# Optimization experiments

Measured on AMD Instinct MI355X. Metric: run time of the kernel, lower is better.

## Reference

```python
import jax, jax.numpy as jnp
import numpy as np

# --- constants from loss_param_dict (fallback norm_info: means=0, stds=1 -> denorm is identity) ---
A_DIV, A_NS, A_BC = 0.3, 0.3, 0.3
A_LOSS = 1.0 - A_DIV - A_NS - A_BC
SCALE_BASE, SCALE_DIV, SCALE_NS, SCALE_BC = 300000.0, 1e-05, 0.01, 1.0
SX, SY = 1.2 / 127, 0.8 / 127  # spacing along axis 2 (x) and axis 1 (y)
RHO, MU = 1.0, 1.0
H, W = 128, 128
IN_TOP = H // 2 + H // 16 + 1  # 73
IN_BOT = H // 2 - H // 16 - 1  # 55
NORM_MEAN = np.array([0.0, 0.0, 0.0, 0.0], dtype=np.float32)
NORM_STD = np.array([1.0, 1.0, 1.0, 1.0], dtype=np.float32)


def grad_axis(f, h, axis):
    """torch.gradient: 2nd-order central interior, 1st-order one-sided edges."""
    f = jnp.moveaxis(f, axis, -1)
    left = (f[..., 1:2] - f[..., 0:1]) / h
    interior = (f[..., 2:] - f[..., :-2]) / (2.0 * h)
    right = (f[..., -1:] - f[..., -2:-1]) / h
    g = jnp.concatenate([left, interior, right], axis=-1)
    return jnp.moveaxis(g, -1, axis)


def setup_inputs() -> dict:
    key = jax.random.key(0)
    k1, k2, k3 = jax.random.split(key, 3)
    B = 256
    return {
        "inputs": jax.random.normal(k1, (B, 1, H, W), dtype=jnp.float32),
        "outputs": jax.random.normal(k2, (B, 3, H, W), dtype=jnp.float32),
        "targets": jax.random.normal(k3, (B, 3, H, W), dtype=jnp.float32),
    }


def reference(inputs, outputs, targets):
    # base MSE loss (reduction='sum')
    loss_base = jnp.sum((outputs - targets) ** 2) / SCALE_BASE

    # denormalisation (norm_info fallback: identity, but kept for faithfulness)
    in_ch = inputs.shape[1]
    mean = jnp.asarray(NORM_MEAN)
    std = jnp.asarray(NORM_STD)
    inp = inputs * std[:in_ch][None, :, None, None] + mean[:in_ch][None, :, None, None]
    out = outputs * std[in_ch:][None, :, None, None] + mean[in_ch:][None, :, None, None]

    # boundary residual pieces (on full, un-cropped denormalised outputs)
    pieces = [
        out[:, 1, IN_BOT:IN_TOP, 0].ravel() - 0.01,
        out[:, 0, IN_BOT:IN_TOP, -1].ravel(),
    ]
    for ch in (1, 2):
        for idx in (0, -1):
            pieces += [
                out[:, ch, idx, :].ravel(),
                out[:, ch, IN_TOP:, idx].ravel(),
                out[:, ch, 0:IN_BOT, idx].ravel(),
            ]
    boundary = jnp.concatenate(pieces)

    # interior crop [B, C, 126, 126]
    i_loc = inp[:, :, 1 : H - 1, 1 : W - 1]
    o_loc = out[:, :, 1 : H - 1, 1 : W - 1]

    p, u, v = o_loc[:, 0], o_loc[:, 1], o_loc[:, 2]  # [B,126,126]
    alpha = i_loc[:, 0]

    dp_dx, dp_dy = grad_axis(p, SX, 2), grad_axis(p, SY, 1)
    du_dx, du_dy = grad_axis(u, SX, 2), grad_axis(u, SY, 1)
    dv_dx, dv_dy = grad_axis(v, SX, 2), grad_axis(v, SY, 1)
    du_dxx = grad_axis(du_dx, SX, 2)
    du_dyy = grad_axis(du_dy, SY, 1)
    dv_dxx = grad_axis(dv_dx, SX, 2)
    dv_dyy = grad_axis(dv_dy, SY, 1)

    # continuity residual
    loss_cont = jnp.mean((du_dx + dv_dy) ** 2) / SCALE_DIV

    # Navier-Stokes residual
    x_res = u * du_dx + v * du_dy + dp_dx / RHO - MU * (du_dxx + du_dyy) / RHO + alpha * u / RHO
    y_res = u * dv_dx + v * dv_dy + dp_dy / RHO - MU * (dv_dxx + dv_dyy) / RHO + alpha * v / RHO
    mse_ns = (jnp.mean(x_res**2, axis=(1, 2)) + jnp.mean(y_res**2, axis=(1, 2))).mean() / 2.0
    loss_ns = mse_ns / SCALE_NS

    # boundary residual
    loss_bc = jnp.mean(boundary**2) / SCALE_BC

    return A_LOSS * loss_base + A_DIV * loss_cont + A_NS * loss_ns + A_BC * loss_bc
```

## Files before the change

### kernel.cpp

```cpp
#include <hip/hip_runtime.h>


#define HH 128
#define WW 128
#define NI 126
#define NBLK 4096

template <int I> __device__ __forceinline__ float gc(const float4& f) {
    if constexpr (I == 0) return f.x;
    else if constexpr (I == 1) return f.y;
    else if constexpr (I == 2) return f.z;
    else return f.w;
}

template <int IDX>
__device__ __forceinline__ float xsel(const float4& l, const float4& m, const float4& r) {
    if constexpr (IDX < 4) return gc<IDX>(l);
    else if constexpr (IDX < 8) return gc<IDX - 4>(m);
    else return gc<IDX - 8>(r);
}

__device__ __forceinline__ float grad1s(float m1, float a0, float p1, int i,
                                        float inv_h, float inv_2h) {
    if (i == 0) return (p1 - a0) * inv_h;
    if (i == NI - 1) return (a0 - m1) * inv_h;
    return (p1 - m1) * inv_2h;
}

__device__ __forceinline__ float grad2s(float m2, float m1, float a0, float p1, float p2,
                                        int i, float inv_h, float inv_2h) {
    if (i == 0) {
        const float d1 = (p2 - a0) * inv_2h, d0 = (p1 - a0) * inv_h;
        return (d1 - d0) * inv_h;
    }
    if (i == 1) {
        const float d1 = (p2 - a0) * inv_2h, dm1 = (a0 - m1) * inv_h;
        return (d1 - dm1) * inv_2h;
    }
    if (i == NI - 1) {
        const float d0 = (a0 - m1) * inv_h, dm1 = (a0 - m2) * inv_2h;
        return (d0 - dm1) * inv_h;
    }
    if (i == NI - 2) {
        const float d1 = (p1 - a0) * inv_h, dm1 = (a0 - m2) * inv_2h;
        return (d1 - dm1) * inv_2h;
    }
    return (p2 - 2.f * a0 + m2) * inv_2h * inv_2h;
}

struct Acc { float base, bc, cont, ns; };

template <int Q>
__device__ __forceinline__ void do_pixel(
    int r, int c0, bool midrow,
    const float4& uxl, const float4& uxm, const float4& uxr,
    const float4& uym2, const float4& uym1, const float4& uyp1, const float4& uyp2,
    const float4& vxl, const float4& vxm, const float4& vxr,
    const float4& vym2, const float4& vym1, const float4& vyp1, const float4& vyp2,
    const float4& pxl, const float4& pxm, const float4& pxr,
    const float4& pym1, const float4& pyp1,
    const float4& t0, const float4& t1, const float4& t2, const float4& av,
    Acc& acc) {
    const int c = c0 + Q;
    const float u0 = xsel<Q + 4>(uxl, uxm, uxr);
    const float v0 = xsel<Q + 4>(vxl, vxm, vxr);
    const float p0 = xsel<Q + 4>(pxl, pxm, pxr);

    {
        const float d0 = p0 - gc<Q>(t0);
        const float d1 = u0 - gc<Q>(t1);
        const float d2 = v0 - gc<Q>(t2);
        acc.base += d0 * d0 + d1 * d1 + d2 * d2;
    }
    if (c == 0 && midrow) { const float d = u0 - 0.01f; acc.bc += d * d; }
    if (c == WW - 1 && midrow) { acc.bc += p0 * p0; }
    if (r == 0 || r == HH - 1) { acc.bc += u0 * u0 + v0 * v0; }
    if ((c == 0 || c == WW - 1) && !midrow) { acc.bc += u0 * u0 + v0 * v0; }

    if (r >= 1 && r <= HH - 2 && c >= 1 && c <= WW - 2) {
        const int ic = c - 1, ir = r - 1;
        const float inv_sx = 127.0f / 1.2f, inv_2sx = 127.0f / 2.4f;
        const float inv_sy = 127.0f / 0.8f, inv_2sy = 127.0f / 1.6f;

        const float uxm2 = xsel<Q + 2>(uxl, uxm, uxr), uxm1 = xsel<Q + 3>(uxl, uxm, uxr);
        const float uxp1 = xsel<Q + 5>(uxl, uxm, uxr), uxp2 = xsel<Q + 6>(uxl, uxm, uxr);
        const float vxm2 = xsel<Q + 2>(vxl, vxm, vxr), vxm1 = xsel<Q + 3>(vxl, vxm, vxr);
        const float vxp1 = xsel<Q + 5>(vxl, vxm, vxr), vxp2 = xsel<Q + 6>(vxl, vxm, vxr);
        const float pxm1 = xsel<Q + 3>(pxl, pxm, pxr), pxp1 = xsel<Q + 5>(pxl, pxm, pxr);
        const float uym2s = gc<Q>(uym2), uym1s = gc<Q>(uym1);
        const float uyp1s = gc<Q>(uyp1), uyp2s = gc<Q>(uyp2);
        const float vym2s = gc<Q>(vym2), vym1s = gc<Q>(vym1);
        const float vyp1s = gc<Q>(vyp1), vyp2s = gc<Q>(vyp2);
        const float pym1s = gc<Q>(pym1), pyp1s = gc<Q>(pyp1);

        const float du_dx = grad1s(uxm1, u0, uxp1, ic, inv_sx, inv_2sx);
        const float du_dy = grad1s(uym1s, u0, uyp1s, ir, inv_sy, inv_2sy);
        const float dv_dx = grad1s(vxm1, v0, vxp1, ic, inv_sx, inv_2sx);
        const float dv_dy = grad1s(vym1s, v0, vyp1s, ir, inv_sy, inv_2sy);
        const float dp_dx = grad1s(pxm1, p0, pxp1, ic, inv_sx, inv_2sx);
        const float dp_dy = grad1s(pym1s, p0, pyp1s, ir, inv_sy, inv_2sy);
        const float du_dxx = grad2s(uxm2, uxm1, u0, uxp1, uxp2, ic, inv_sx, inv_2sx);
        const float du_dyy = grad2s(uym2s, uym1s, u0, uyp1s, uyp2s, ir, inv_sy, inv_2sy);
        const float dv_dxx = grad2s(vxm2, vxm1, v0, vxp1, vxp2, ic, inv_sx, inv_2sx);
        const float dv_dyy = grad2s(vym2s, vym1s, v0, vyp1s, vyp2s, ir, inv_sy, inv_2sy);

        const float alpha = gc<Q>(av);
        const float dvg = du_dx + dv_dy;
        acc.cont += dvg * dvg;
        const float xr_ = u0 * du_dx + v0 * du_dy + dp_dx - (du_dxx + du_dyy) + alpha * u0;
        const float yr_ = u0 * dv_dx + v0 * dv_dy + dp_dy - (dv_dxx + dv_dyy) + alpha * v0;
        acc.ns += xr_ * xr_ + yr_ * yr_;
    }
}

__global__ __launch_bounds__(256, 4) void physics_loss_kernel(
    const float* __restrict__ inp, const float* __restrict__ out,
    const float* __restrict__ tgt, double* __restrict__ ws) {
    const int tid = threadIdx.x;
    const int grp = tid & 31;
    const int rloc = tid >> 5;
    const int bid = ((blockIdx.x & 7) << 9) | (blockIdx.x >> 3);
    const int b = bid >> 4;
    const int r = ((bid & 15) << 3) | rloc;
    const int c0 = grp << 2;

    const float* O = out + (size_t)b * 3 * HH * WW;
    const float* T = tgt + (size_t)b * 3 * HH * WW;
    const float* A = inp + (size_t)b * HH * WW;
    const float* P = O;
    const float* U = O + HH * WW;
    const float* V = O + 2 * HH * WW;

    const int gl = grp == 0 ? 0 : grp - 1;
    const int gr = grp == 31 ? 31 : grp + 1;
    const int rm2 = r < 2 ? 0 : r - 2;
    const int rm1 = r < 1 ? 0 : r - 1;
    const int rp1 = r > 126 ? 127 : r + 1;
    const int rp2 = r > 125 ? 127 : r + 2;

    auto ld = [&](const float* base, int row, int gg) {
        return reinterpret_cast<const float4*>(base + row * WW)[gg];
    };

    const float4 uxl = ld(U, r, gl), uxm = ld(U, r, grp), uxr = ld(U, r, gr);
    const float4 uym2 = ld(U, rm2, grp), uym1 = ld(U, rm1, grp);
    const float4 uyp1 = ld(U, rp1, grp), uyp2 = ld(U, rp2, grp);
    const float4 vxl = ld(V, r, gl), vxm = ld(V, r, grp), vxr = ld(V, r, gr);
    const float4 vym2 = ld(V, rm2, grp), vym1 = ld(V, rm1, grp);
    const float4 vyp1 = ld(V, rp1, grp), vyp2 = ld(V, rp2, grp);
    const float4 pxl = ld(P, r, gl), pxm = ld(P, r, grp), pxr = ld(P, r, gr);
    const float4 pym1 = ld(P, rm1, grp), pyp1 = ld(P, rp1, grp);
    const float4 t0 = ld(T, r, grp);
    const float4 t1 = ld(T + HH * WW, r, grp);
    const float4 t2 = ld(T + 2 * HH * WW, r, grp);
    const float4 av = ld(A, r, grp);
    __builtin_amdgcn_sched_barrier(0);

    const bool midrow = (r >= 55 && r < 73);
    Acc acc = {0.f, 0.f, 0.f, 0.f};

    do_pixel<0>(r, c0, midrow, uxl, uxm, uxr, uym2, uym1, uyp1, uyp2,
                vxl, vxm, vxr, vym2, vym1, vyp1, vyp2,
                pxl, pxm, pxr, pym1, pyp1, t0, t1, t2, av, acc);
    do_pixel<1>(r, c0, midrow, uxl, uxm, uxr, uym2, uym1, uyp1, uyp2,
                vxl, vxm, vxr, vym2, vym1, vyp1, vyp2,
                pxl, pxm, pxr, pym1, pyp1, t0, t1, t2, av, acc);
    do_pixel<2>(r, c0, midrow, uxl, uxm, uxr, uym2, uym1, uyp1, uyp2,
                vxl, vxm, vxr, vym2, vym1, vyp1, vyp2,
                pxl, pxm, pxr, pym1, pyp1, t0, t1, t2, av, acc);
    do_pixel<3>(r, c0, midrow, uxl, uxm, uxr, uym2, uym1, uyp1, uyp2,
                vxl, vxm, vxr, vym2, vym1, vyp1, vyp2,
                pxl, pxm, pxr, pym1, pyp1, t0, t1, t2, av, acc);

    float a_base = acc.base, a_bc = acc.bc, a_cont = acc.cont, a_ns = acc.ns;
    #pragma unroll
    for (int off = 32; off > 0; off >>= 1) {
        a_base += __shfl_down(a_base, off);
        a_bc   += __shfl_down(a_bc, off);
        a_cont += __shfl_down(a_cont, off);
        a_ns   += __shfl_down(a_ns, off);
    }
    __shared__ float red[4][4];
    const int wave = tid >> 6, lane = tid & 63;
    if (lane == 0) {
        red[wave][0] = a_base; red[wave][1] = a_bc;
        red[wave][2] = a_cont; red[wave][3] = a_ns;
    }
    __syncthreads();
    if (tid == 0) {
        double b0 = 0, b1 = 0, b2 = 0, b3 = 0;
        #pragma unroll
        for (int w = 0; w < 4; ++w) {
            b0 += red[w][0]; b1 += red[w][1]; b2 += red[w][2]; b3 += red[w][3];
        }
        double* slot = ws + (size_t)bid * 4;
        slot[0] = b0; slot[1] = b1; slot[2] = b2; slot[3] = b3;
    }
}

__global__ __launch_bounds__(256) void finalize_kernel(const double* __restrict__ ws,
                                                       float* __restrict__ out) {
    const int tid = threadIdx.x;
    double a0 = 0, a1 = 0, a2 = 0, a3 = 0;
    for (int b = tid; b < NBLK; b += 256) {
        const double* p = ws + (size_t)b * 4;
        a0 += p[0]; a1 += p[1]; a2 += p[2]; a3 += p[3];
    }
    #pragma unroll
    for (int off = 32; off > 0; off >>= 1) {
        a0 += __shfl_down(a0, off);
        a1 += __shfl_down(a1, off);
        a2 += __shfl_down(a2, off);
        a3 += __shfl_down(a3, off);
    }
    __shared__ double red[4][4];
    const int wave = tid >> 6, lane = tid & 63;
    if (lane == 0) {
        red[wave][0] = a0; red[wave][1] = a1; red[wave][2] = a2; red[wave][3] = a3;
    }
    __syncthreads();
    if (tid == 0) {
        double b0 = 0, b1 = 0, b2 = 0, b3 = 0;
        #pragma unroll
        for (int w = 0; w < 4; ++w) {
            b0 += red[w][0]; b1 += red[w][1]; b2 += red[w][2]; b3 += red[w][3];
        }
        const double loss_base = b0 / 300000.0;
        const double loss_cont = b2 / (256.0 * 126.0 * 126.0) / 1e-5;
        const double loss_ns   = b3 / (2.0 * 256.0 * 126.0 * 126.0) / 0.01;
        const double loss_bc   = b1 / (256.0 * 988.0);
        out[0] = (float)(0.10000000000000009 * loss_base +
                         0.3 * (loss_cont + loss_ns + loss_bc));
    }
}

extern "C" void kernel_launch(void* const* d_in, const int* in_sizes, int n_in,
                              void* d_out, int out_size, void* d_ws, size_t ws_size,
                              hipStream_t stream) {
    const float* inp = (const float*)d_in[0];
    const float* out = (const float*)d_in[1];
    const float* tgt = (const float*)d_in[2];
    float* o = (float*)d_out;
    double* ws = (double*)d_ws;

    hipLaunchKernelGGL(physics_loss_kernel, dim3(NBLK), dim3(256), 0, stream,
                       inp, out, tgt, ws);
    hipLaunchKernelGGL(finalize_kernel, dim3(1), dim3(256), 0, stream, ws, o);
}
```

Measured before the change: 31.87 us.

## Stage u/v/p stencil rows into LDS via global_load_lds instead of redundant global loads

Each block now copies the 12 u rows, 12 v rows and 10 p rows it needs (including halo) into a shared-memory tile using async global-to-LDS loads. Neighbour values then come from LDS, replacing the 19 overlapping float4 global loads per thread. The goal is less redundant global/L2 traffic and fewer vector registers. The cost is an extra __syncthreads and LDS pressure, and the occupancy hint in launch_bounds is dropped.

```diff
diff --git a/kernel.cpp b/kernel.cpp
--- a/kernel.cpp
+++ b/kernel.cpp
@@ -5,6 +5,9 @@
 #define WW 128
 #define NI 126
 #define NBLK 4096
+
+#define AS1C(p) ((const __attribute__((address_space(1))) void*)(p))
+#define AS3(p)  ((__attribute__((address_space(3))) void*)(p))
 
 template <int I> __device__ __forceinline__ float gc(const float4& f) {
     if constexpr (I == 0) return f.x;
@@ -113,7 +116,7 @@
     }
 }
 
-__global__ __launch_bounds__(256, 4) void physics_loss_kernel(
+__global__ __launch_bounds__(256) void physics_loss_kernel(
     const float* __restrict__ inp, const float* __restrict__ out,
     const float* __restrict__ tgt, double* __restrict__ ws) {
     const int tid = threadIdx.x;
@@ -121,8 +124,11 @@
     const int rloc = tid >> 5;
     const int bid = ((blockIdx.x & 7) << 9) | (blockIdx.x >> 3);
     const int b = bid >> 4;
-    const int r = ((bid & 15) << 3) | rloc;
+    const int r0 = (bid & 15) << 3;
+    const int r = r0 | rloc;
     const int c0 = grp << 2;
+    const int lane = tid & 63;
+    const int wv = tid >> 6;
 
     const float* O = out + (size_t)b * 3 * HH * WW;
     const float* T = tgt + (size_t)b * 3 * HH * WW;
@@ -131,30 +137,47 @@
     const float* U = O + HH * WW;
     const float* V = O + 2 * HH * WW;
 
-    const int gl = grp == 0 ? 0 : grp - 1;
-    const int gr = grp == 31 ? 31 : grp + 1;
-    const int rm2 = r < 2 ? 0 : r - 2;
-    const int rm1 = r < 1 ? 0 : r - 1;
-    const int rp1 = r > 126 ? 127 : r + 1;
-    const int rp2 = r > 125 ? 127 : r + 2;
+    __shared__ float tile[34][128];
 
     auto ld = [&](const float* base, int row, int gg) {
         return reinterpret_cast<const float4*>(base + row * WW)[gg];
     };
-
-    const float4 uxl = ld(U, r, gl), uxm = ld(U, r, grp), uxr = ld(U, r, gr);
-    const float4 uym2 = ld(U, rm2, grp), uym1 = ld(U, rm1, grp);
-    const float4 uyp1 = ld(U, rp1, grp), uyp2 = ld(U, rp2, grp);
-    const float4 vxl = ld(V, r, gl), vxm = ld(V, r, grp), vxr = ld(V, r, gr);
-    const float4 vym2 = ld(V, rm2, grp), vym1 = ld(V, rm1, grp);
-    const float4 vyp1 = ld(V, rp1, grp), vyp2 = ld(V, rp2, grp);
-    const float4 pxl = ld(P, r, gl), pxm = ld(P, r, grp), pxr = ld(P, r, gr);
-    const float4 pym1 = ld(P, rm1, grp), pyp1 = ld(P, rp1, grp);
     const float4 t0 = ld(T, r, grp);
     const float4 t1 = ld(T + HH * WW, r, grp);
     const float4 t2 = ld(T + 2 * HH * WW, r, grp);
     const float4 av = ld(A, r, grp);
-    __builtin_amdgcn_sched_barrier(0);
+
+    const int lsub = lane >> 5;
+    const int lcol = (lane & 31) << 2;
+    for (int ci = wv; ci < 17; ci += 4) {
+        const float* src;
+        int grow;
+        if (ci < 6)       { src = U; grow = r0 - 2 + ci * 2 + lsub; }
+        else if (ci < 12) { src = V; grow = r0 - 2 + (ci - 6) * 2 + lsub; }
+        else              { src = P; grow = r0 - 1 + (ci - 12) * 2 + lsub; }
+        grow = grow < 0 ? 0 : (grow > 127 ? 127 : grow);
+        const float* gaddr = src + grow * WW + lcol;
+        __builtin_amdgcn_global_load_lds(AS1C(gaddr),
+                                         AS3((char*)&tile[0][0] + ci * 1024),
+                                         16, 0, 0);
+    }
+    __syncthreads();
+
+    const int gl = grp == 0 ? 0 : grp - 1;
+    const int gr = grp == 31 ? 31 : grp + 1;
+    auto lrow = [&](int row) { return reinterpret_cast<const float4*>(&tile[row][0]); };
+    const float4 uym2 = lrow(rloc)[grp],     uym1 = lrow(rloc + 1)[grp];
+    const float4 uxl  = lrow(rloc + 2)[gl],  uxm  = lrow(rloc + 2)[grp];
+    const float4 uxr  = lrow(rloc + 2)[gr];
+    const float4 uyp1 = lrow(rloc + 3)[grp], uyp2 = lrow(rloc + 4)[grp];
+    const float4 vym2 = lrow(12 + rloc)[grp],     vym1 = lrow(12 + rloc + 1)[grp];
+    const float4 vxl  = lrow(12 + rloc + 2)[gl],  vxm  = lrow(12 + rloc + 2)[grp];
+    const float4 vxr  = lrow(12 + rloc + 2)[gr];
+    const float4 vyp1 = lrow(12 + rloc + 3)[grp], vyp2 = lrow(12 + rloc + 4)[grp];
+    const float4 pym1 = lrow(24 + rloc)[grp];
+    const float4 pxl  = lrow(24 + rloc + 1)[gl],  pxm  = lrow(24 + rloc + 1)[grp];
+    const float4 pxr  = lrow(24 + rloc + 1)[gr];
+    const float4 pyp1 = lrow(24 + rloc + 2)[grp];
 
     const bool midrow = (r >= 55 && r < 73);
     Acc acc = {0.f, 0.f, 0.f, 0.f};
@@ -181,10 +204,9 @@
         a_ns   += __shfl_down(a_ns, off);
     }
     __shared__ float red[4][4];
-    const int wave = tid >> 6, lane = tid & 63;
     if (lane == 0) {
-        red[wave][0] = a_base; red[wave][1] = a_bc;
-        red[wave][2] = a_cont; red[wave][3] = a_ns;
+        red[wv][0] = a_base; red[wv][1] = a_bc;
+        red[wv][2] = a_cont; red[wv][3] = a_ns;
     }
     __syncthreads();
     if (tid == 0) {
```

Measured after the change: 37.75 us. 1.18x slower.
